# Kernel optimization log

Measured on AMD Instinct MI355X. Metric: run time of the kernel, lower is better.

The kernel has to match this reference:

```python
import jax, jax.numpy as jnp
import numpy as np
import math

N_HEAD = 16
K_SPARSE = 64

def setup_inputs() -> dict:
    key = jax.random.key(0)
    ks = jax.random.split(key, 12)
    B, T, C = 1, 2048, 1024
    s = 0.02
    return {
        "x":   jax.random.normal(ks[0], (B, T, C), jnp.float32),
        "Wq":  jax.random.normal(ks[1], (C, C), jnp.float32) * s,
        "bq":  jax.random.normal(ks[2], (C,), jnp.float32) * s,
        "Wk":  jax.random.normal(ks[3], (C, C), jnp.float32) * s,
        "bk":  jax.random.normal(ks[4], (C,), jnp.float32) * s,
        "Wv":  jax.random.normal(ks[5], (C, C), jnp.float32) * s,
        "bv":  jax.random.normal(ks[6], (C,), jnp.float32) * s,
        "Wo":  jax.random.normal(ks[7], (C, C), jnp.float32) * s,
        "bo":  jax.random.normal(ks[8], (C,), jnp.float32) * s,
        "Wks": jax.random.normal(ks[9], (C,), jnp.float32) * s,
        "bks": jax.random.normal(ks[10], (), jnp.float32) * s,
    }

def reference(x, Wq, bq, Wk, bk, Wv, bv, Wo, bo, Wks, bks):
    B, T, C = x.shape
    nh = N_HEAD
    hs = C // nh
    k_val = min(K_SPARSE, T)

    # projections -> (B, nh, T, hs)   (torch Linear: x @ W.T + b)
    q = (x @ Wq.T + bq).reshape(B, T, nh, hs).transpose(0, 2, 1, 3)
    k = (x @ Wk.T + bk).reshape(B, T, nh, hs).transpose(0, 2, 1, 3)
    v = (x @ Wv.T + bv).reshape(B, T, nh, hs).transpose(0, 2, 1, 3)

    # key scorer: per-token scalar score (B, T)
    key_scores = x @ Wks + bks

    # causal masking of scores, then per-query top-k key selection
    pos = jnp.arange(T)
    causal = pos[None, :] <= pos[:, None]                      # (T, T), True where key<=query
    masked = jnp.where(causal[None], key_scores[:, None, :], -jnp.inf)  # (B, T, T)
    _, top_k_idx = jax.lax.top_k(masked, k_val)                # (B, T, k)
    top_k_idx = jnp.minimum(top_k_idx, pos[None, :, None])     # clamp to <= query pos

    # gather sparse keys/values: (B, nh, T, k, hs)
    bi = jnp.arange(B)[:, None, None, None]
    hi = jnp.arange(nh)[None, :, None, None]
    gi = top_k_idx[:, None, :, :]                              # (B, 1, T, k)
    sparse_k = k[bi, hi, gi]                                   # (B, nh, T, k, hs)
    sparse_v = v[bi, hi, gi]

    scale = 1.0 / math.sqrt(hs)
    logits = jnp.einsum('bhtd,bhtkd->bhtk', q, sparse_k) * scale
    probs = jax.nn.softmax(logits, axis=-1)
    out = jnp.einsum('bhtk,bhtkd->bhtd', probs, sparse_v)      # (B, nh, T, hs)
    out = out.transpose(0, 2, 1, 3).reshape(B, T, C)
    return out @ Wo.T + bo
```

## Files before the change

### kernel.cpp

```cpp
#include <hip/hip_runtime.h>
#include <hip/hip_bf16.h>
#include <cstdint>
#include <cstddef>

#define T_DIM 2048
#define C_DIM 1024
#define NH 16
#define HS 64
#define KSP 64

#define GBM 128
#define GBN 64
#define GBK 128
#define OBM 64
#define OBN 64

#define ATB 16
#define USLOT (KSP + ATB - 1)
#define KSTR 66

typedef short short8 __attribute__((ext_vector_type(8)));
typedef float f32x4 __attribute__((ext_vector_type(4)));
typedef _Float16 half2_t __attribute__((ext_vector_type(2)));

__device__ __forceinline__ unsigned short f2bfu(float f) {
  unsigned u = __builtin_bit_cast(unsigned, f);
  unsigned r = (u + 0x7fffu + ((u >> 16) & 1u)) >> 16;
  return (unsigned short)r;
}
__device__ __forceinline__ unsigned short f2h(float f) {
  _Float16 h = (_Float16)f;
  return __builtin_bit_cast(unsigned short, h);
}
__device__ __forceinline__ float bflo(unsigned u) {
  return __builtin_bit_cast(float, u << 16);
}
__device__ __forceinline__ float bfhi(unsigned u) {
  return __builtin_bit_cast(float, u & 0xffff0000u);
}

__device__ __forceinline__ float dot2h(unsigned kbits, unsigned qbits, float acc) {
#if __has_builtin(__builtin_amdgcn_fdot2)
  return __builtin_amdgcn_fdot2(__builtin_bit_cast(half2_t, kbits),
                                __builtin_bit_cast(half2_t, qbits), acc, false);
#else
  half2_t kk = __builtin_bit_cast(half2_t, kbits);
  half2_t qq = __builtin_bit_cast(half2_t, qbits);
  return acc + (float)kk.x * (float)qq.x + (float)kk.y * (float)qq.y;
#endif
}

#define GLOAD_LDS16(gp, lp)                                                  \
  __builtin_amdgcn_global_load_lds(                                          \
      (const __attribute__((address_space(1))) void*)(gp),                   \
      (__attribute__((address_space(3))) void*)(lp), 16, 0, 0)

#define NSCORE (T_DIM / 4)
#define NCONV ((T_DIM * C_DIM + 4 * C_DIM * C_DIM) / 4 / 256)
__global__ __launch_bounds__(256) void convert_scores_kernel(
    const float* __restrict__ x, const float* __restrict__ Wq,
    const float* __restrict__ Wk, const float* __restrict__ Wv,
    const float* __restrict__ Wo, const float* __restrict__ Wks,
    const float* __restrict__ bks,
    unsigned short* __restrict__ xb, unsigned short* __restrict__ Wqb,
    unsigned short* __restrict__ Wkb, unsigned short* __restrict__ Wvb,
    unsigned short* __restrict__ Wob, float* __restrict__ scores) {
  if (blockIdx.x < NSCORE) {
    const int t = blockIdx.x * 4 + (threadIdx.x >> 6);
    const int lane = threadIdx.x & 63;
    const float* xrow = x + (size_t)t * C_DIM;
    float acc = 0.f;
    #pragma unroll 4
    for (int i = lane; i < C_DIM; i += 64)
      acc += xrow[i] * Wks[i];
    #pragma unroll
    for (int o = 32; o; o >>= 1) acc += __shfl_xor(acc, o);
    if (lane == 0) scores[t] = acc + bks[0];
    return;
  }
  const int i = (blockIdx.x - NSCORE) * 256 + threadIdx.x;
  const int NX4 = T_DIM * C_DIM / 4;
  const int NW4 = C_DIM * C_DIM / 4;
  const float* src;
  unsigned short* dst;
  int j = i;
  if (j < NX4) { src = x; dst = xb; }
  else {
    j -= NX4;
    int w = j / NW4;
    j -= w * NW4;
    src = (w == 0) ? Wq : (w == 1) ? Wk : (w == 2) ? Wv : Wo;
    dst = (w == 0) ? Wqb : (w == 1) ? Wkb : (w == 2) ? Wvb : Wob;
  }
  float4 f = reinterpret_cast<const float4*>(src)[j];
  ushort4 o;
  o.x = f2bfu(f.x); o.y = f2bfu(f.y); o.z = f2bfu(f.z); o.w = f2bfu(f.w);
  reinterpret_cast<ushort4*>(dst)[j] = o;
}

__device__ __forceinline__ void gemm_body_128x64(
    const unsigned short* __restrict__ A, const unsigned short* __restrict__ W,
    f32x4 acc[4][2], int bm, int bn, int tid,
    unsigned short* As, unsigned short* Ws) {
  const int w = tid >> 6, lane = tid & 63;
  const int quad = lane >> 4, r = lane & 15;
  const int wm = (w >> 1) * 64, wn = (w & 1) * 32;
  const int sub = lane >> 4;
  const int c = lane & 15;
  const unsigned short* Arow[8];
  const unsigned short* Wrow[4];
  #pragma unroll
  for (int i = 0; i < 8; ++i) {
    const int row = w * 32 + i * 4 + sub;
    Arow[i] = A + (size_t)(bm * GBM + row) * C_DIM + ((c ^ (row & 7)) * 8);
  }
  #pragma unroll
  for (int i = 0; i < 4; ++i) {
    const int row = w * 16 + i * 4 + sub;
    Wrow[i] = W + (size_t)(bn * GBN + row) * C_DIM + ((c ^ (row & 7)) * 8);
  }
  for (int kb = 0; kb < C_DIM; kb += GBK) {
    #pragma unroll
    for (int i = 0; i < 8; ++i)
      GLOAD_LDS16(Arow[i] + kb, &As[(w * 32 + i * 4) * GBK]);
    #pragma unroll
    for (int i = 0; i < 4; ++i)
      GLOAD_LDS16(Wrow[i] + kb, &Ws[(w * 16 + i * 4) * GBK]);
    __syncthreads();
    #pragma unroll
    for (int ks = 0; ks < 4; ++ks) {
      const int pc = ((ks * 4 + quad) ^ (r & 7)) * 8;
      short8 af[4], bfr[2];
      #pragma unroll
      for (int mi = 0; mi < 4; ++mi)
        af[mi] = *reinterpret_cast<const short8*>(&As[(wm + mi * 16 + r) * GBK + pc]);
      #pragma unroll
      for (int ni = 0; ni < 2; ++ni)
        bfr[ni] = *reinterpret_cast<const short8*>(&Ws[(wn + ni * 16 + r) * GBK + pc]);
      #pragma unroll
      for (int mi = 0; mi < 4; ++mi)
        #pragma unroll
        for (int ni = 0; ni < 2; ++ni)
          acc[mi][ni] = __builtin_amdgcn_mfma_f32_16x16x32_bf16(af[mi], bfr[ni], acc[mi][ni], 0, 0, 0);
    }
    __syncthreads();
  }
}

#define NRANK (T_DIM / 4)
__global__ __launch_bounds__(256) void gemm_qkv_rank_kernel(
    const unsigned short* __restrict__ A,
    const unsigned short* __restrict__ Wq, const unsigned short* __restrict__ Wk,
    const unsigned short* __restrict__ Wv,
    const float* __restrict__ bq, const float* __restrict__ bk,
    const float* __restrict__ bv,
    unsigned short* __restrict__ qo, unsigned short* __restrict__ ko,
    unsigned short* __restrict__ vo,
    const float* __restrict__ scores, int* __restrict__ sorted_idx) {
  __shared__ unsigned short lds[(GBM + GBN) * GBK];
  const int tid = threadIdx.x;
  if (blockIdx.x < NRANK) {
    float* ss = reinterpret_cast<float*>(lds);
    for (int j = tid; j < T_DIM; j += 256) ss[j] = scores[j];
    __syncthreads();
    const int w = tid >> 6, lane = tid & 63;
    const int i = blockIdx.x * 4 + w;
    const float si = ss[i];
    int rank = 0;
    #pragma unroll
    for (int step = 0; step < T_DIM / 64; ++step) {
      const int j = step * 64 + lane;
      const float sj = ss[j];
      rank += (int)((sj > si) || (sj == si && j < i));
    }
    #pragma unroll
    for (int o = 32; o; o >>= 1) rank += __shfl_xor(rank, o);
    if (lane == 0) sorted_idx[rank] = i;
    return;
  }
  const int bid = blockIdx.x - NRANK;
  const int per = (T_DIM / GBM) * (C_DIM / GBN);
  const int which = bid / per;
  const int rem = bid % per;
  const int bm = rem / (C_DIM / GBN);
  const int bn = rem % (C_DIM / GBN);
  const unsigned short* W = (which == 0) ? Wq : (which == 1) ? Wk : Wv;
  const float* bias = (which == 0) ? bq : (which == 1) ? bk : bv;
  unsigned short* out = (which == 0) ? qo : (which == 1) ? ko : vo;
  f32x4 acc[4][2] = {};
  gemm_body_128x64(A, W, acc, bm, bn, tid, lds, lds + GBM * GBK);
  const int w = tid >> 6, lane = tid & 63;
  const int quad = lane >> 4, r = lane & 15;
  const int wm = (w >> 1) * 64, wn = (w & 1) * 32;
  #pragma unroll
  for (int mi = 0; mi < 4; ++mi) {
    #pragma unroll
    for (int ni = 0; ni < 2; ++ni) {
      const int col = bn * GBN + wn + ni * 16 + r;
      const float bf = bias[col];
      #pragma unroll
      for (int i = 0; i < 4; ++i) {
        const int row = bm * GBM + wm + mi * 16 + quad * 4 + i;
        const float val = acc[mi][ni][i] + bf;
        out[(size_t)row * C_DIM + col] = (which == 2) ? f2bfu(val) : f2h(val);
      }
    }
  }
}

__device__ __forceinline__ void gemm_body_64x64(
    const unsigned short* __restrict__ A, const unsigned short* __restrict__ W,
    f32x4 acc[2][2], int bm, int bn, int tid) {
  __shared__ unsigned short As[OBM * GBK];
  __shared__ unsigned short Ws[OBN * GBK];
  const int w = tid >> 6, lane = tid & 63;
  const int quad = lane >> 4, r = lane & 15;
  const int wm = (w >> 1) * 32, wn = (w & 1) * 32;
  const int sub = lane >> 4;
  const int c = lane & 15;
  const unsigned short* Arow[4];
  const unsigned short* Wrow[4];
  #pragma unroll
  for (int i = 0; i < 4; ++i) {
    const int row = w * 16 + i * 4 + sub;
    Arow[i] = A + (size_t)(bm * OBM + row) * C_DIM + ((c ^ (row & 7)) * 8);
    Wrow[i] = W + (size_t)(bn * OBN + row) * C_DIM + ((c ^ (row & 7)) * 8);
  }
  for (int kb = 0; kb < C_DIM; kb += GBK) {
    #pragma unroll
    for (int i = 0; i < 4; ++i)
      GLOAD_LDS16(Arow[i] + kb, &As[(w * 16 + i * 4) * GBK]);
    #pragma unroll
    for (int i = 0; i < 4; ++i)
      GLOAD_LDS16(Wrow[i] + kb, &Ws[(w * 16 + i * 4) * GBK]);
    __syncthreads();
    #pragma unroll
    for (int ks = 0; ks < 4; ++ks) {
      const int pc = ((ks * 4 + quad) ^ (r & 7)) * 8;
      short8 af[2], bfr[2];
      #pragma unroll
      for (int mi = 0; mi < 2; ++mi)
        af[mi] = *reinterpret_cast<const short8*>(&As[(wm + mi * 16 + r) * GBK + pc]);
      #pragma unroll
      for (int ni = 0; ni < 2; ++ni)
        bfr[ni] = *reinterpret_cast<const short8*>(&Ws[(wn + ni * 16 + r) * GBK + pc]);
      #pragma unroll
      for (int mi = 0; mi < 2; ++mi)
        #pragma unroll
        for (int ni = 0; ni < 2; ++ni)
          acc[mi][ni] = __builtin_amdgcn_mfma_f32_16x16x32_bf16(af[mi], bfr[ni], acc[mi][ni], 0, 0, 0);
    }
    __syncthreads();
  }
}

__global__ __launch_bounds__(256) void gemm_o_f32_kernel(
    const unsigned short* __restrict__ A, const unsigned short* __restrict__ W,
    const float* __restrict__ bias, float* __restrict__ out) {
  const int tid = threadIdx.x;
  const int bm = blockIdx.x / (C_DIM / OBN);
  const int bn = blockIdx.x % (C_DIM / OBN);
  f32x4 acc[2][2] = {};
  gemm_body_64x64(A, W, acc, bm, bn, tid);
  const int w = tid >> 6, lane = tid & 63;
  const int quad = lane >> 4, r = lane & 15;
  const int wm = (w >> 1) * 32, wn = (w & 1) * 32;
  #pragma unroll
  for (int mi = 0; mi < 2; ++mi) {
    #pragma unroll
    for (int ni = 0; ni < 2; ++ni) {
      const int col = bn * OBN + wn + ni * 16 + r;
      const float bf = bias[col];
      #pragma unroll
      for (int i = 0; i < 4; ++i) {
        const int row = bm * OBM + wm + mi * 16 + quad * 4 + i;
        out[(size_t)row * C_DIM + col] = acc[mi][ni][i] + bf;
      }
    }
  }
}

__global__ __launch_bounds__(256) void attn_kernel(
    const unsigned short* __restrict__ q, const unsigned short* __restrict__ k,
    const unsigned short* __restrict__ v, const int* __restrict__ sorted_idx,
    unsigned short* __restrict__ attn_out) {
  __shared__ unsigned short Kl[USLOT * KSTR];
  __shared__ unsigned short Vl[USLOT * KSTR];
  __shared__ short map_s[T_DIM];
  __shared__ short rows_tab[ATB][KSP];
  __shared__ short urows[USLOT];
  const int tb = blockIdx.x >> 4;
  const int h = blockIdx.x & (NH - 1);
  const int t0 = tb * ATB;
  const int tid = threadIdx.x;
  const int w = tid >> 6, lane = tid & 63;
  const int c8 = lane & 7;
  const int ksub = lane >> 3;
  uint4 qr[ATB / 4];
  #pragma unroll
  for (int li = 0; li < ATB / 4; ++li) {
    const int t = t0 + w * (ATB / 4) + li;
    qr[li] = *reinterpret_cast<const uint4*>(q + (size_t)t * C_DIM + h * HS + 8 * c8);
  }
  const unsigned long long lt_mask = (1ull << lane) - 1ull;
  for (int li = 0; li < ATB / 4; ++li) {
    const int tt = w * (ATB / 4) + li;
    const int t = t0 + tt;
    if (t <= 63) {
      rows_tab[tt][lane] = (short)((lane < t) ? lane : t);
    } else {
      int count = 0;
      for (int c = 0; c < T_DIM / 64 && count < KSP; ++c) {
        int s = sorted_idx[c * 64 + lane];
        s = (s < 0) ? 0 : (s > T_DIM - 1 ? T_DIM - 1 : s);
        const bool ok = (s <= t);
        const unsigned long long mm = __ballot(ok);
        const int pos = count + __popcll(mm & lt_mask);
        if (ok && pos < KSP) rows_tab[tt][pos] = (short)s;
        count += __popcll(mm);
      }
    }
    if (w == 0 && li == 0) {
      const int r0 = rows_tab[0][lane];
      map_s[r0] = (short)lane;
      urows[lane] = (short)r0;
      if (lane < ATB - 1) {
        map_s[t0 + 1 + lane] = (short)(KSP + lane);
        urows[KSP + lane] = (short)(t0 + 1 + lane);
      }
    }
  }
  __syncthreads();
  {
    const int e8 = tid & 7;
    for (int s = tid >> 3; s < USLOT; s += 32) {
      const int row = urows[s];
      const size_t gb = (size_t)row * C_DIM + h * HS + e8 * 8;
      *reinterpret_cast<uint4*>(&Kl[s * KSTR + e8 * 8]) =
          *reinterpret_cast<const uint4*>(k + gb);
      *reinterpret_cast<uint4*>(&Vl[s * KSTR + e8 * 8]) =
          *reinterpret_cast<const uint4*>(v + gb);
    }
  }
  __syncthreads();
  for (int li = 0; li < ATB / 4; ++li) {
    const int tt = w * (ATB / 4) + li;
    const int t = t0 + tt;
    const uint4 qraw = qr[li];
    int slot[8];
    #pragma unroll
    for (int jj = 0; jj < 8; ++jj)
      slot[jj] = map_s[rows_tab[tt][8 * jj + ksub]];
    float l[8];
    #pragma unroll
    for (int jj = 0; jj < 8; ++jj) {
      const uint4 raw =
          *reinterpret_cast<const uint4*>(&Kl[slot[jj] * KSTR + 8 * c8]);
      float pl = dot2h(raw.x, qraw.x, 0.f);
      pl = dot2h(raw.y, qraw.y, pl);
      pl = dot2h(raw.z, qraw.z, pl);
      pl = dot2h(raw.w, qraw.w, pl);
      pl *= 0.125f;
      pl += __shfl_xor(pl, 1);
      pl += __shfl_xor(pl, 2);
      pl += __shfl_xor(pl, 4);
      l[jj] = pl;
    }
    float m = l[0];
    #pragma unroll
    for (int jj = 1; jj < 8; ++jj) m = fmaxf(m, l[jj]);
    m = fmaxf(m, __shfl_xor(m, 8));
    m = fmaxf(m, __shfl_xor(m, 16));
    m = fmaxf(m, __shfl_xor(m, 32));
    float sum = 0.f;
    #pragma unroll
    for (int jj = 0; jj < 8; ++jj) {
      l[jj] = __expf(l[jj] - m);
      sum += l[jj];
    }
    sum += __shfl_xor(sum, 8);
    sum += __shfl_xor(sum, 16);
    sum += __shfl_xor(sum, 32);
    const float rs = 1.0f / sum;
    float a[8] = {0.f, 0.f, 0.f, 0.f, 0.f, 0.f, 0.f, 0.f};
    #pragma unroll
    for (int jj = 0; jj < 8; ++jj) {
      const uint4 raw =
          *reinterpret_cast<const uint4*>(&Vl[slot[jj] * KSTR + 8 * c8]);
      const float p = l[jj] * rs;
      a[0] += p * bflo(raw.x); a[1] += p * bfhi(raw.x);
      a[2] += p * bflo(raw.y); a[3] += p * bfhi(raw.y);
      a[4] += p * bflo(raw.z); a[5] += p * bfhi(raw.z);
      a[6] += p * bflo(raw.w); a[7] += p * bfhi(raw.w);
    }
    #pragma unroll
    for (int o = 8; o <= 32; o <<= 1) {
      #pragma unroll
      for (int z = 0; z < 8; ++z) a[z] += __shfl_xor(a[z], o);
    }
    if (ksub == 0) {
      ushort4 o0, o1;
      o0.x = f2bfu(a[0]); o0.y = f2bfu(a[1]); o0.z = f2bfu(a[2]); o0.w = f2bfu(a[3]);
      o1.x = f2bfu(a[4]); o1.y = f2bfu(a[5]); o1.z = f2bfu(a[6]); o1.w = f2bfu(a[7]);
      ushort4* dst =
          reinterpret_cast<ushort4*>(attn_out + (size_t)t * C_DIM + h * HS + 8 * c8);
      dst[0] = o0;
      dst[1] = o1;
    }
  }
}

extern "C" void kernel_launch(void* const* d_in, const int* in_sizes, int n_in,
                              void* d_out, int out_size, void* d_ws, size_t ws_size,
                              hipStream_t stream) {
  const float* x   = (const float*)d_in[0];
  const float* Wq  = (const float*)d_in[1];
  const float* bq  = (const float*)d_in[2];
  const float* Wk  = (const float*)d_in[3];
  const float* bk  = (const float*)d_in[4];
  const float* Wv  = (const float*)d_in[5];
  const float* bv  = (const float*)d_in[6];
  const float* Wo  = (const float*)d_in[7];
  const float* bo  = (const float*)d_in[8];
  const float* Wks = (const float*)d_in[9];
  const float* bks = (const float*)d_in[10];
  float* out = (float*)d_out;

  char* ws = (char*)d_ws;
  size_t off = 0;
  float* scores = (float*)(ws + off); off += 8192;
  int*   sorted = (int*)(ws + off);   off += 8192;
  unsigned short* xb  = (unsigned short*)(ws + off); off += (size_t)T_DIM * C_DIM * 2;
  unsigned short* Wqb = (unsigned short*)(ws + off); off += (size_t)C_DIM * C_DIM * 2;
  unsigned short* Wkb = (unsigned short*)(ws + off); off += (size_t)C_DIM * C_DIM * 2;
  unsigned short* Wvb = (unsigned short*)(ws + off); off += (size_t)C_DIM * C_DIM * 2;
  unsigned short* Wob = (unsigned short*)(ws + off); off += (size_t)C_DIM * C_DIM * 2;
  unsigned short* qb  = (unsigned short*)(ws + off); off += (size_t)T_DIM * C_DIM * 2;
  unsigned short* kb  = (unsigned short*)(ws + off); off += (size_t)T_DIM * C_DIM * 2;
  unsigned short* vb  = (unsigned short*)(ws + off); off += (size_t)T_DIM * C_DIM * 2;
  unsigned short* ab  = xb;

  convert_scores_kernel<<<NSCORE + NCONV, 256, 0, stream>>>(
      x, Wq, Wk, Wv, Wo, Wks, bks, xb, Wqb, Wkb, Wvb, Wob, scores);

  gemm_qkv_rank_kernel<<<NRANK + 3 * (T_DIM / GBM) * (C_DIM / GBN), 256, 0,
                         stream>>>(
      xb, Wqb, Wkb, Wvb, bq, bk, bv, qb, kb, vb, scores, sorted);

  attn_kernel<<<(T_DIM / ATB) * NH, 256, 0, stream>>>(qb, kb, vb, sorted, ab);

  gemm_o_f32_kernel<<<(T_DIM / OBM) * (C_DIM / OBN), 256, 0, stream>>>(
      ab, Wob, bo, out);
}
```

Measured before the change: 160.9 us.

## Precompute per-query top-k selection once and use DPP reductions in attention

Moves the per-query causal top-k row selection out of the attention kernel into a separate select kernel, which writes a compact table of selected key rows. Before, all 16 heads recomputed the selection for every query block. The attention kernel now reads that table from global memory. Several cross-lane reductions are switched from shuffles to DPP row operations, and the query loop is unrolled by two. The cost is one extra kernel launch plus the write and read of the small selection table.

```diff
diff --git a/kernel.cpp b/kernel.cpp
--- a/kernel.cpp
+++ b/kernel.cpp
@@ -19,6 +19,11 @@
 #define USLOT (KSP + ATB - 1)
 #define KSTR 66
 
+#define DPP_XOR1 0xB1
+#define DPP_XOR2 0x4E
+#define DPP_HMIRR 0x141
+#define DPP_ROR8 0x128
+
 typedef short short8 __attribute__((ext_vector_type(8)));
 typedef float f32x4 __attribute__((ext_vector_type(4)));
 typedef _Float16 half2_t __attribute__((ext_vector_type(2)));
@@ -37,6 +42,19 @@
 }
 __device__ __forceinline__ float bfhi(unsigned u) {
   return __builtin_bit_cast(float, u & 0xffff0000u);
+}
+
+template <int CTRL>
+__device__ __forceinline__ float dpp_add_f(float x) {
+  const int xi = __builtin_bit_cast(int, x);
+  const int y = __builtin_amdgcn_update_dpp(xi, xi, CTRL, 0xF, 0xF, true);
+  return x + __builtin_bit_cast(float, y);
+}
+template <int CTRL>
+__device__ __forceinline__ float dpp_max_f(float x) {
+  const int xi = __builtin_bit_cast(int, x);
+  const int y = __builtin_amdgcn_update_dpp(xi, xi, CTRL, 0xF, 0xF, true);
+  return fmaxf(x, __builtin_bit_cast(float, y));
 }
 
 __device__ __forceinline__ float dot2h(unsigned kbits, unsigned qbits, float acc) {
@@ -280,14 +298,36 @@
   }
 }
 
+__global__ __launch_bounds__(256) void select_kernel(
+    const int* __restrict__ sorted_idx, unsigned short* __restrict__ sel) {
+  const int tid = threadIdx.x;
+  const int w = tid >> 6, lane = tid & 63;
+  const int t = blockIdx.x * 4 + w;
+  unsigned short* dst = sel + (size_t)t * KSP;
+  if (t <= 63) {
+    dst[lane] = (unsigned short)((lane < t) ? lane : t);
+    return;
+  }
+  const unsigned long long lt_mask = (1ull << lane) - 1ull;
+  int count = 0;
+  for (int c = 0; c < T_DIM / 64 && count < KSP; ++c) {
+    int s = sorted_idx[c * 64 + lane];
+    s = (s < 0) ? 0 : (s > T_DIM - 1 ? T_DIM - 1 : s);
+    const bool ok = (s <= t);
+    const unsigned long long mm = __ballot(ok);
+    const int pos = count + __popcll(mm & lt_mask);
+    if (ok && pos < KSP) dst[pos] = (unsigned short)s;
+    count += __popcll(mm);
+  }
+}
+
 __global__ __launch_bounds__(256) void attn_kernel(
     const unsigned short* __restrict__ q, const unsigned short* __restrict__ k,
-    const unsigned short* __restrict__ v, const int* __restrict__ sorted_idx,
+    const unsigned short* __restrict__ v, const unsigned short* __restrict__ sel,
     unsigned short* __restrict__ attn_out) {
   __shared__ unsigned short Kl[USLOT * KSTR];
   __shared__ unsigned short Vl[USLOT * KSTR];
   __shared__ short map_s[T_DIM];
-  __shared__ short rows_tab[ATB][KSP];
   __shared__ short urows[USLOT];
   const int tb = blockIdx.x >> 4;
   const int h = blockIdx.x & (NH - 1);
@@ -302,33 +342,14 @@
     const int t = t0 + w * (ATB / 4) + li;
     qr[li] = *reinterpret_cast<const uint4*>(q + (size_t)t * C_DIM + h * HS + 8 * c8);
   }
-  const unsigned long long lt_mask = (1ull << lane) - 1ull;
-  for (int li = 0; li < ATB / 4; ++li) {
-    const int tt = w * (ATB / 4) + li;
-    const int t = t0 + tt;
-    if (t <= 63) {
-      rows_tab[tt][lane] = (short)((lane < t) ? lane : t);
-    } else {
-      int count = 0;
-      for (int c = 0; c < T_DIM / 64 && count < KSP; ++c) {
-        int s = sorted_idx[c * 64 + lane];
-        s = (s < 0) ? 0 : (s > T_DIM - 1 ? T_DIM - 1 : s);
-        const bool ok = (s <= t);
-        const unsigned long long mm = __ballot(ok);
-        const int pos = count + __popcll(mm & lt_mask);
-        if (ok && pos < KSP) rows_tab[tt][pos] = (short)s;
-        count += __popcll(mm);
-      }
-    }
-    if (w == 0 && li == 0) {
-      const int r0 = rows_tab[0][lane];
-      map_s[r0] = (short)lane;
-      urows[lane] = (short)r0;
-      if (lane < ATB - 1) {
-        map_s[t0 + 1 + lane] = (short)(KSP + lane);
-        urows[KSP + lane] = (short)(t0 + 1 + lane);
-      }
-    }
+  if (tid < KSP) {
+    const int r0 = sel[(size_t)t0 * KSP + tid];
+    map_s[r0] = (short)tid;
+    urows[tid] = (short)r0;
+  } else if (tid < USLOT) {
+    const int row = t0 + 1 + (tid - KSP);
+    map_s[row] = (short)tid;
+    urows[tid] = (short)row;
   }
   __syncthreads();
   {
@@ -343,14 +364,16 @@
     }
   }
   __syncthreads();
+  #pragma unroll 2
   for (int li = 0; li < ATB / 4; ++li) {
     const int tt = w * (ATB / 4) + li;
     const int t = t0 + tt;
     const uint4 qraw = qr[li];
+    const unsigned short* __restrict__ selt = sel + (size_t)t * KSP;
     int slot[8];
     #pragma unroll
     for (int jj = 0; jj < 8; ++jj)
-      slot[jj] = map_s[rows_tab[tt][8 * jj + ksub]];
+      slot[jj] = map_s[selt[8 * jj + ksub]];
     float l[8];
     #pragma unroll
     for (int jj = 0; jj < 8; ++jj) {
@@ -361,15 +384,15 @@
       pl = dot2h(raw.z, qraw.z, pl);
       pl = dot2h(raw.w, qraw.w, pl);
       pl *= 0.125f;
-      pl += __shfl_xor(pl, 1);
-      pl += __shfl_xor(pl, 2);
-      pl += __shfl_xor(pl, 4);
+      pl = dpp_add_f<DPP_XOR1>(pl);
+      pl = dpp_add_f<DPP_XOR2>(pl);
+      pl = dpp_add_f<DPP_HMIRR>(pl);
       l[jj] = pl;
     }
     float m = l[0];
     #pragma unroll
     for (int jj = 1; jj < 8; ++jj) m = fmaxf(m, l[jj]);
-    m = fmaxf(m, __shfl_xor(m, 8));
+    m = dpp_max_f<DPP_ROR8>(m);
     m = fmaxf(m, __shfl_xor(m, 16));
     m = fmaxf(m, __shfl_xor(m, 32));
     float sum = 0.f;
@@ -378,7 +401,7 @@
       l[jj] = __expf(l[jj] - m);
       sum += l[jj];
     }
-    sum += __shfl_xor(sum, 8);
+    sum = dpp_add_f<DPP_ROR8>(sum);
     sum += __shfl_xor(sum, 16);
     sum += __shfl_xor(sum, 32);
     const float rs = 1.0f / sum;
@@ -394,10 +417,11 @@
       a[6] += p * bflo(raw.w); a[7] += p * bfhi(raw.w);
     }
     #pragma unroll
-    for (int o = 8; o <= 32; o <<= 1) {
-      #pragma unroll
-      for (int z = 0; z < 8; ++z) a[z] += __shfl_xor(a[z], o);
-    }
+    for (int z = 0; z < 8; ++z) a[z] = dpp_add_f<DPP_ROR8>(a[z]);
+    #pragma unroll
+    for (int z = 0; z < 8; ++z) a[z] += __shfl_xor(a[z], 16);
+    #pragma unroll
+    for (int z = 0; z < 8; ++z) a[z] += __shfl_xor(a[z], 32);
     if (ksub == 0) {
       ushort4 o0, o1;
       o0.x = f2bfu(a[0]); o0.y = f2bfu(a[1]); o0.z = f2bfu(a[2]); o0.w = f2bfu(a[3]);
@@ -430,6 +454,7 @@
   size_t off = 0;
   float* scores = (float*)(ws + off); off += 8192;
   int*   sorted = (int*)(ws + off);   off += 8192;
+  unsigned short* selb = (unsigned short*)(ws + off); off += (size_t)T_DIM * KSP * 2;
   unsigned short* xb  = (unsigned short*)(ws + off); off += (size_t)T_DIM * C_DIM * 2;
   unsigned short* Wqb = (unsigned short*)(ws + off); off += (size_t)C_DIM * C_DIM * 2;
   unsigned short* Wkb = (unsigned short*)(ws + off); off += (size_t)C_DIM * C_DIM * 2;
@@ -447,7 +472,9 @@
                          stream>>>(
       xb, Wqb, Wkb, Wvb, bq, bk, bv, qb, kb, vb, scores, sorted);
 
-  attn_kernel<<<(T_DIM / ATB) * NH, 256, 0, stream>>>(qb, kb, vb, sorted, ab);
+  select_kernel<<<T_DIM / 4, 256, 0, stream>>>(sorted, selb);
+
+  attn_kernel<<<(T_DIM / ATB) * NH, 256, 0, stream>>>(qb, kb, vb, selb, ab);
 
   gemm_o_f32_kernel<<<(T_DIM / OBM) * (C_DIM / OBN), 256, 0, stream>>>(
       ab, Wob, bo, out);
```

New measurement: 160.8 us. Within noise of the previous version (-0.1%).
